# Optimization experiments

Hardware: AMD Instinct MI355X
Metric: run time of the kernel (lower is better)

## Reference

```python
import jax, jax.numpy as jnp
import numpy as np

WIN = 8          # window size
SHIFT = 4        # shift size
NH = 6           # num heads
HD = 32          # head dim
DIM = NH * HD    # 192
SCALE = HD ** (-0.5)
B, H, W = 4, 256, 256

def _rel_index():
    coords = np.stack(np.meshgrid(np.arange(WIN), np.arange(WIN), indexing='ij'))  # (2,w,w)
    cf = coords.reshape(2, -1)                       # (2, w*w)
    rel = (cf[:, :, None] - cf[:, None, :]).transpose(1, 2, 0)  # (w*w, w*w, 2)
    rel[..., 0] += WIN - 1
    rel[..., 1] += WIN - 1
    rel[..., 0] *= 2 * WIN - 1
    return rel.sum(-1)                               # (w*w, w*w) int

REL_IDX = _rel_index()

def _shift_mask(h, w):
    # same construction as get_shift_mask (static shapes -> plain numpy)
    m = np.zeros((h, w))
    cnt = 0
    for hs in (slice(0, -WIN), slice(-WIN, -SHIFT), slice(-SHIFT, None)):
        for ws in (slice(0, -WIN), slice(-WIN, -SHIFT), slice(-SHIFT, None)):
            m[hs, ws] = cnt
            cnt += 1
    # mask_window_partition -> (nW, win_seq)
    m = m.reshape(h // WIN, WIN, w // WIN, WIN).transpose(0, 2, 1, 3).reshape(-1, WIN * WIN)
    am = m[:, None, :] - m[:, :, None]               # unsqueeze(1) - unsqueeze(2)
    return np.where(am != 0, -100.0, 0.0).astype(np.float32)  # (nW, ws^2, ws^2)

SHIFT_MASK = _shift_mask(H, W)

def setup_inputs() -> dict:
    key = jax.random.key(0)
    k1, k2 = jax.random.split(key)
    x = jax.random.normal(k1, (B, 3 * DIM, H, W), dtype=jnp.float32)
    rpb_table = jax.random.normal(k2, ((2 * WIN - 1) ** 2, NH), dtype=jnp.float32) * 0.02
    return {"x": x, "rpb_table": rpb_table}

def reference(x, rpb_table):
    b, _, h, w = x.shape
    nwh, nww = h // WIN, w // WIN
    nw = nwh * nww
    ws2 = WIN * WIN
    if SHIFT > 0:
        x = jnp.roll(x, shift=(-SHIFT, -SHIFT), axis=(2, 3))
    # winP: (B, 3*C, H, W) -> (3, B*nW, NH, ws^2, HD)
    qkv = x.reshape(b, 3, NH, HD, nwh, WIN, nww, WIN)
    qkv = qkv.transpose(1, 0, 4, 6, 2, 5, 7, 3).reshape(3, b * nw, NH, ws2, HD)
    q, k, v = qkv[0], qkv[1], qkv[2]
    att = jnp.einsum('wnqd,wnkd->wnqk', q, k) * SCALE   # (B*nW, NH, ws^2, ws^2)
    rpb = rpb_table[REL_IDX.reshape(-1)].reshape(ws2, ws2, NH).transpose(2, 0, 1)
    att = att + rpb[None]
    if SHIFT > 0:
        mask = jnp.asarray(SHIFT_MASK)                  # (nW, ws^2, ws^2)
        att = att.reshape(b, nw, NH, ws2, ws2) + mask[None, :, None]
        att = att.reshape(b * nw, NH, ws2, ws2)
    att = jax.nn.softmax(att, axis=-1)
    out = jnp.einsum('wnqk,wnkd->wnqd', att, v)         # (B*nW, NH, ws^2, HD)
    # winR: back to (B, NH*HD, H, W)
    out = out.reshape(b, nwh, nww, NH, WIN, WIN, HD)
    out = out.transpose(0, 3, 6, 1, 4, 2, 5).reshape(b, NH * HD, h, w)
    if SHIFT > 0:
        out = jnp.roll(out, shift=(SHIFT, SHIFT), axis=(2, 3))
    return out
```

## Files before the change

### kernel.cpp

```cpp
#include <hip/hip_runtime.h>

#define NH 6
#define HWSZ 65536
#define SCALE 0.17677669529663687f

typedef __attribute__((ext_vector_type(8)))  short short8t;
typedef __attribute__((ext_vector_type(16))) float f32x16;
typedef __attribute__((ext_vector_type(4)))  unsigned int uint4t;

__device__ __forceinline__ unsigned int pack2(float a, float b) {
  return (__float_as_uint(a) >> 16) | (__float_as_uint(b) & 0xffff0000u);
}
__device__ __forceinline__ float btrunc_f(float a) {
  return __uint_as_float(__float_as_uint(a) & 0xffff0000u);
}
__device__ __forceinline__ float resid(float a) { return a - btrunc_f(a); }

__device__ __forceinline__ void split8(const float (&f)[8], short8t& h, short8t& l) {
  uint4t hw, lw;
#pragma unroll
  for (int i = 0; i < 4; ++i) {
    const float a = f[2*i], c = f[2*i+1];
    hw[i] = pack2(a, c);
    lw[i] = pack2(resid(a), resid(c));
  }
  h = __builtin_bit_cast(short8t, hw);
  l = __builtin_bit_cast(short8t, lw);
}

__global__ __launch_bounds__(64, 2)
void swin_attn_mfma(const float* __restrict__ x,
                    const float* __restrict__ rpb,
                    float* __restrict__ out) {
  __shared__ float Vt[2048];
  __shared__ float rpb_s[232];

  const int raw = (int)blockIdx.x;
  const int lid = (raw & 7) * 3072 + (raw >> 3);
  const int ww = lid & 31;
  int t = lid >> 5;
  const int nh = t % NH; t /= NH;
  const int wh = t & 31;
  const int b  = t >> 5;

  const int lane = (int)threadIdx.x;
  const int lo = lane & 31, hi = lane >> 5;

  {
    const int dly = lane >> 4;
    const int chp = (lane & 15) >> 1;
    const int off0 = (lane & 1) * 4;
    const int s0e = ((chp ^ dly) << 3) + off0;
    const int s0o = ((chp ^ (4 + dly)) << 3) + off0;
    const size_t cb = (size_t)(b * 576 + 384 + nh * 32 + dly) * HWSZ;
    const float* gve = x + cb + (size_t)(((wh*8+4+(s0e>>3)) & 255) * 256 + ((ww*8+4+(s0e&7)) & 255));
    const float* gvo = x + cb + (size_t)(((wh*8+4+(s0o>>3)) & 255) * 256 + ((ww*8+4+(s0o&7)) & 255));
#pragma unroll
    for (int i = 0; i < 8; ++i) {
      const float* src = (i & 1) ? gvo : gve;
      __builtin_amdgcn_global_load_lds(
          (const __attribute__((address_space(1))) void*)(src + (size_t)i * 4 * HWSZ),
          (__attribute__((address_space(3))) void*)(&Vt[i * 256]), 16, 0, 0);
    }
  }
  for (int r = lane; r < 225; r += 64) rpb_s[r] = rpb[r * NH + nh];

  const int iy = lo >> 3, ix = lo & 7;
  const int sh0 = (wh*8 + 4 + iy) & 255;
  const int sh1 = (wh*8 + 8 + iy) & 255;
  const int sw  = (ww*8 + 4 + ix) & 255;
  const size_t pix0 = (size_t)sh0 * 256 + sw;
  const size_t pix1 = (size_t)sh1 * 256 + sw;
  const size_t qcb = (size_t)(b * 576 + nh * 32) * HWSZ;
  const size_t kcb = qcb + (size_t)192 * HWSZ;

  short8t qh[2][2], ql[2][2], kh[2][2], kl[2][2];
#pragma unroll
  for (int ks = 0; ks < 2; ++ks) {
#pragma unroll
    for (int tt = 0; tt < 2; ++tt) {
      const size_t pp = tt ? pix1 : pix0;
      float f[8], g[8];
#pragma unroll
      for (int e = 0; e < 8; ++e) {
        const size_t dof = (size_t)(ks*16 + hi*8 + e) * HWSZ;
        f[e] = x[qcb + dof + pp];
        g[e] = x[kcb + dof + pp];
      }
      split8(f, qh[ks][tt], ql[ks][tt]);
      split8(g, kh[ks][tt], kl[ks][tt]);
    }
  }

  f32x16 acc[2][2];
#pragma unroll
  for (int mt = 0; mt < 2; ++mt)
#pragma unroll
    for (int nt = 0; nt < 2; ++nt)
#pragma unroll
      for (int r = 0; r < 16; ++r) acc[mt][nt][r] = 0.f;

#pragma unroll
  for (int ks = 0; ks < 2; ++ks)
#pragma unroll
    for (int mt = 0; mt < 2; ++mt)
#pragma unroll
      for (int nt = 0; nt < 2; ++nt) {
        acc[mt][nt] = __builtin_amdgcn_mfma_f32_32x32x16_bf16(kh[ks][mt], qh[ks][nt], acc[mt][nt], 0, 0, 0);
        acc[mt][nt] = __builtin_amdgcn_mfma_f32_32x32x16_bf16(kh[ks][mt], ql[ks][nt], acc[mt][nt], 0, 0, 0);
        acc[mt][nt] = __builtin_amdgcn_mfma_f32_32x32x16_bf16(kl[ks][mt], qh[ks][nt], acc[mt][nt], 0, 0, 0);
      }

  __syncthreads();

  const bool eh = (wh == 31), ew = (ww == 31);
  float mrow[2] = {-1e30f, -1e30f};
#pragma unroll
  for (int nt = 0; nt < 2; ++nt) {
    const int qyy = 4*nt + iy;
    const int rq = (eh ? 1 + (qyy >> 2) : 0) * 3 + (ew ? 1 + (ix >> 2) : 0);
    const int qoff = (qyy + 7) * 15 + (ix + 7);
#pragma unroll
    for (int mt = 0; mt < 2; ++mt)
#pragma unroll
      for (int r = 0; r < 16; ++r) {
        const int ky = 4*mt + (r >> 2);
        const int kx = 4*hi + (r & 3);
        float a = fmaf(acc[mt][nt][r], SCALE, rpb_s[qoff - ky*15 - kx]);
        const int rk = (eh ? 1 + (ky >> 2) : 0) * 3 + (ew ? 1 + (kx >> 2) : 0);
        a += (rk == rq) ? 0.f : -100.f;
        acc[mt][nt][r] = a;
        mrow[nt] = fmaxf(mrow[nt], a);
      }
  }
  mrow[0] = fmaxf(mrow[0], __shfl_xor(mrow[0], 32));
  mrow[1] = fmaxf(mrow[1], __shfl_xor(mrow[1], 32));

  float sum0 = 0.f, sum1 = 0.f;
#pragma unroll
  for (int mt = 0; mt < 2; ++mt)
#pragma unroll
    for (int r = 0; r < 16; ++r) {
      const float p0 = __expf(acc[mt][0][r] - mrow[0]);
      const float p1 = __expf(acc[mt][1][r] - mrow[1]);
      acc[mt][0][r] = p0; sum0 += p0;
      acc[mt][1][r] = p1; sum1 += p1;
    }
  sum0 += __shfl_xor(sum0, 32);
  sum1 += __shfl_xor(sum1, 32);
  const float rs0 = 1.f / sum0, rs1 = 1.f / sum1;

  f32x16 oacc[2];
#pragma unroll
  for (int r = 0; r < 16; ++r) { oacc[0][r] = 0.f; oacc[1][r] = 0.f; }

#pragma unroll
  for (int ks2 = 0; ks2 < 4; ++ks2) {
    const int mt = ks2 >> 1, bs = (ks2 & 1) * 8;
    float vf[8];
    {
      const int chp = (2*ks2 + hi) ^ (lo & 7);
      const float4 v0 = *(const float4*)&Vt[lo*64 + chp*8];
      const float4 v1 = *(const float4*)&Vt[lo*64 + chp*8 + 4];
      vf[0]=v0.x; vf[1]=v0.y; vf[2]=v0.z; vf[3]=v0.w;
      vf[4]=v1.x; vf[5]=v1.y; vf[6]=v1.z; vf[7]=v1.w;
    }
    short8t vh, vl; split8(vf, vh, vl);
#pragma unroll
    for (int nt = 0; nt < 2; ++nt) {
      const float a0 = acc[mt][nt][bs+0], a1 = acc[mt][nt][bs+1];
      const float a2 = acc[mt][nt][bs+2], a3 = acc[mt][nt][bs+3];
      const float b0 = acc[mt][nt][bs+4], b1 = acc[mt][nt][bs+5];
      const float b2 = acc[mt][nt][bs+6], b3 = acc[mt][nt][bs+7];
      const unsigned int Ah0 = pack2(a0, a1), Ah1 = pack2(a2, a3);
      const unsigned int Bh0 = pack2(b0, b1), Bh1 = pack2(b2, b3);
      const unsigned int Al0 = pack2(resid(a0), resid(a1)), Al1 = pack2(resid(a2), resid(a3));
      const unsigned int Bl0 = pack2(resid(b0), resid(b1)), Bl1 = pack2(resid(b2), resid(b3));
      const unsigned int xAh0 = __shfl_xor(Ah0, 32), xAh1 = __shfl_xor(Ah1, 32);
      const unsigned int xBh0 = __shfl_xor(Bh0, 32), xBh1 = __shfl_xor(Bh1, 32);
      const unsigned int xAl0 = __shfl_xor(Al0, 32), xAl1 = __shfl_xor(Al1, 32);
      const unsigned int xBl0 = __shfl_xor(Bl0, 32), xBl1 = __shfl_xor(Bl1, 32);
      uint4t wh4, wl4;
      wh4[0] = hi ? xBh0 : Ah0;  wh4[1] = hi ? xBh1 : Ah1;
      wh4[2] = hi ? Bh0 : xAh0;  wh4[3] = hi ? Bh1 : xAh1;
      wl4[0] = hi ? xBl0 : Al0;  wl4[1] = hi ? xBl1 : Al1;
      wl4[2] = hi ? Bl0 : xAl0;  wl4[3] = hi ? Bl1 : xAl1;
      const short8t pbh = __builtin_bit_cast(short8t, wh4);
      const short8t pbl = __builtin_bit_cast(short8t, wl4);
      oacc[nt] = __builtin_amdgcn_mfma_f32_32x32x16_bf16(vh, pbh, oacc[nt], 0, 0, 0);
      oacc[nt] = __builtin_amdgcn_mfma_f32_32x32x16_bf16(vh, pbl, oacc[nt], 0, 0, 0);
      oacc[nt] = __builtin_amdgcn_mfma_f32_32x32x16_bf16(vl, pbh, oacc[nt], 0, 0, 0);
    }
  }

  const size_t ocb = (size_t)(b * 192 + nh * 32) * HWSZ;
#pragma unroll
  for (int r = 0; r < 16; ++r) {
    const int d = 4*hi + (r & 3) + 8*(r >> 2);
    out[ocb + (size_t)d * HWSZ + pix0] = oacc[0][r] * rs0;
    out[ocb + (size_t)d * HWSZ + pix1] = oacc[1][r] * rs1;
  }
}

extern "C" void kernel_launch(void* const* d_in, const int* in_sizes, int n_in,
                              void* d_out, int out_size, void* d_ws, size_t ws_size,
                              hipStream_t stream) {
  const float* x   = (const float*)d_in[0];
  const float* rpb = (const float*)d_in[1];
  float* out = (float*)d_out;
  dim3 grid(4 * 32 * 32 * NH);
  dim3 block(64);
  hipLaunchKernelGGL(swin_attn_mfma, grid, block, 0, stream, x, rpb, out);
}
```

Before: 1.006 ms.

## Group four adjacent windows per 256-thread block with per-wave V slices

Each block now runs four waves, one per horizontally adjacent window, instead of one 64-thread block per window. Each wave gets its own LDS V slice with a re-swizzled 4-float chunk layout. The block-wide barrier is replaced by a per-wave vmcnt wait, since each wave only reads V it loaded itself. Interior windows also take a fast path that skips the shift-mask computation. The aim is better memory locality, lower per-block launch and barrier overhead, and fewer ALU ops. In exchange each block uses more LDS, and every wave redundantly rewrites the shared rpb table.

Result: faster. 939.8 us (-6.6%).

```diff
diff --git a/kernel.cpp b/kernel.cpp
--- a/kernel.cpp
+++ b/kernel.cpp
@@ -28,39 +28,43 @@
   l = __builtin_bit_cast(short8t, lw);
 }
 
-__global__ __launch_bounds__(64, 2)
-void swin_attn_mfma(const float* __restrict__ x,
-                    const float* __restrict__ rpb,
-                    float* __restrict__ out) {
-  __shared__ float Vt[2048];
+__global__ __launch_bounds__(256, 4)
+void swin_attn_mfma4(const float* __restrict__ x,
+                     const float* __restrict__ rpb,
+                     float* __restrict__ out) {
+  __shared__ float Vt[4][2048];
   __shared__ float rpb_s[232];
 
   const int raw = (int)blockIdx.x;
-  const int lid = (raw & 7) * 3072 + (raw >> 3);
-  const int ww = lid & 31;
-  int t = lid >> 5;
+  const int lid = (raw & 7) * 768 + (raw >> 3);
+  const int wwg = lid & 7;
+  int t = lid >> 3;
   const int nh = t % NH; t /= NH;
   const int wh = t & 31;
   const int b  = t >> 5;
 
-  const int lane = (int)threadIdx.x;
+  const int tid  = (int)threadIdx.x;
+  const int wid  = tid >> 6;
+  const int lane = tid & 63;
+  const int ww   = wwg * 4 + wid;
   const int lo = lane & 31, hi = lane >> 5;
+
+  float* vslice = &Vt[wid][0];
 
   {
     const int dly = lane >> 4;
-    const int chp = (lane & 15) >> 1;
-    const int off0 = (lane & 1) * 4;
-    const int s0e = ((chp ^ dly) << 3) + off0;
-    const int s0o = ((chp ^ (4 + dly)) << 3) + off0;
+    const int sl  = lane & 15;
+    const int se  = (sl ^ dly) << 2;
+    const int so  = (sl ^ (4 + dly)) << 2;
     const size_t cb = (size_t)(b * 576 + 384 + nh * 32 + dly) * HWSZ;
-    const float* gve = x + cb + (size_t)(((wh*8+4+(s0e>>3)) & 255) * 256 + ((ww*8+4+(s0e&7)) & 255));
-    const float* gvo = x + cb + (size_t)(((wh*8+4+(s0o>>3)) & 255) * 256 + ((ww*8+4+(s0o&7)) & 255));
+    const float* gve = x + cb + (size_t)(((wh*8+4+(se>>3)) & 255) * 256 + ((ww*8+4+(se&7)) & 255));
+    const float* gvo = x + cb + (size_t)(((wh*8+4+(so>>3)) & 255) * 256 + ((ww*8+4+(so&7)) & 255));
 #pragma unroll
     for (int i = 0; i < 8; ++i) {
       const float* src = (i & 1) ? gvo : gve;
       __builtin_amdgcn_global_load_lds(
           (const __attribute__((address_space(1))) void*)(src + (size_t)i * 4 * HWSZ),
-          (__attribute__((address_space(3))) void*)(&Vt[i * 256]), 16, 0, 0);
+          (__attribute__((address_space(3))) void*)(&vslice[i * 256]), 16, 0, 0);
     }
   }
   for (int r = lane; r < 225; r += 64) rpb_s[r] = rpb[r * NH + nh];
@@ -111,27 +115,41 @@
         acc[mt][nt] = __builtin_amdgcn_mfma_f32_32x32x16_bf16(kl[ks][mt], qh[ks][nt], acc[mt][nt], 0, 0, 0);
       }
 
-  __syncthreads();
-
   const bool eh = (wh == 31), ew = (ww == 31);
   float mrow[2] = {-1e30f, -1e30f};
-#pragma unroll
-  for (int nt = 0; nt < 2; ++nt) {
-    const int qyy = 4*nt + iy;
-    const int rq = (eh ? 1 + (qyy >> 2) : 0) * 3 + (ew ? 1 + (ix >> 2) : 0);
-    const int qoff = (qyy + 7) * 15 + (ix + 7);
-#pragma unroll
-    for (int mt = 0; mt < 2; ++mt)
-#pragma unroll
-      for (int r = 0; r < 16; ++r) {
-        const int ky = 4*mt + (r >> 2);
-        const int kx = 4*hi + (r & 3);
-        float a = fmaf(acc[mt][nt][r], SCALE, rpb_s[qoff - ky*15 - kx]);
-        const int rk = (eh ? 1 + (ky >> 2) : 0) * 3 + (ew ? 1 + (kx >> 2) : 0);
-        a += (rk == rq) ? 0.f : -100.f;
-        acc[mt][nt][r] = a;
-        mrow[nt] = fmaxf(mrow[nt], a);
-      }
+  if (!eh && !ew) {
+#pragma unroll
+    for (int nt = 0; nt < 2; ++nt) {
+      const int qoff = (4*nt + iy + 7) * 15 + (ix + 7);
+#pragma unroll
+      for (int mt = 0; mt < 2; ++mt)
+#pragma unroll
+        for (int r = 0; r < 16; ++r) {
+          const int koff = (4*mt + (r >> 2)) * 15 + 4*hi + (r & 3);
+          const float a = fmaf(acc[mt][nt][r], SCALE, rpb_s[qoff - koff]);
+          acc[mt][nt][r] = a;
+          mrow[nt] = fmaxf(mrow[nt], a);
+        }
+    }
+  } else {
+#pragma unroll
+    for (int nt = 0; nt < 2; ++nt) {
+      const int qyy = 4*nt + iy;
+      const int rq = (eh ? 1 + (qyy >> 2) : 0) * 3 + (ew ? 1 + (ix >> 2) : 0);
+      const int qoff = (qyy + 7) * 15 + (ix + 7);
+#pragma unroll
+      for (int mt = 0; mt < 2; ++mt)
+#pragma unroll
+        for (int r = 0; r < 16; ++r) {
+          const int ky = 4*mt + (r >> 2);
+          const int kx = 4*hi + (r & 3);
+          float a = fmaf(acc[mt][nt][r], SCALE, rpb_s[qoff - ky*15 - kx]);
+          const int rk = (eh ? 1 + (ky >> 2) : 0) * 3 + (ew ? 1 + (kx >> 2) : 0);
+          a += (rk == rq) ? 0.f : -100.f;
+          acc[mt][nt][r] = a;
+          mrow[nt] = fmaxf(mrow[nt], a);
+        }
+    }
   }
   mrow[0] = fmaxf(mrow[0], __shfl_xor(mrow[0], 32));
   mrow[1] = fmaxf(mrow[1], __shfl_xor(mrow[1], 32));
@@ -150,6 +168,8 @@
   sum1 += __shfl_xor(sum1, 32);
   const float rs0 = 1.f / sum0, rs1 = 1.f / sum1;
 
+  asm volatile("s_waitcnt vmcnt(0)" ::: "memory");
+
   f32x16 oacc[2];
 #pragma unroll
   for (int r = 0; r < 16; ++r) { oacc[0][r] = 0.f; oacc[1][r] = 0.f; }
@@ -159,9 +179,10 @@
     const int mt = ks2 >> 1, bs = (ks2 & 1) * 8;
     float vf[8];
     {
-      const int chp = (2*ks2 + hi) ^ (lo & 7);
-      const float4 v0 = *(const float4*)&Vt[lo*64 + chp*8];
-      const float4 v1 = *(const float4*)&Vt[lo*64 + chp*8 + 4];
+      const int sp0 = ((4*ks2 + 2*hi)     ^ (lo & 7)) * 4;
+      const int sp1 = ((4*ks2 + 2*hi + 1) ^ (lo & 7)) * 4;
+      const float4 v0 = *(const float4*)&vslice[lo*64 + sp0];
+      const float4 v1 = *(const float4*)&vslice[lo*64 + sp1];
       vf[0]=v0.x; vf[1]=v0.y; vf[2]=v0.z; vf[3]=v0.w;
       vf[4]=v1.x; vf[5]=v1.y; vf[6]=v1.z; vf[7]=v1.w;
     }
@@ -208,7 +229,7 @@
   const float* x   = (const float*)d_in[0];
   const float* rpb = (const float*)d_in[1];
   float* out = (float*)d_out;
-  dim3 grid(4 * 32 * 32 * NH);
-  dim3 block(64);
-  hipLaunchKernelGGL(swin_attn_mfma, grid, block, 0, stream, x, rpb, out);
-}
+  dim3 grid(4 * 32 * NH * 8);
+  dim3 block(256);
+  hipLaunchKernelGGL(swin_attn_mfma4, grid, block, 0, stream, x, rpb, out);
+}
```
